# Optimization experiments

Hardware: AMD Instinct MI355X
Metric: run time of the kernel (lower is better)

The kernel has to match this reference:

```python
import jax, jax.numpy as jnp
import numpy as np

B, N, K, D, H, L = 2, 2048, 256, 768, 256, 64
REL_PROP = 3
NUM_BUCKETS = 64


def _pair_scores(u, dist_feat, left_w, left_b, right_w, right_b, out_w, out_b):
    # OptFFpairs-style pairwise scorer: left(u)_i + right(u)_j + dist_emb -> relu -> out
    left = jnp.einsum('bkd,hd->bkh', u, left_w) + left_b    # [B,K,H]
    right = jnp.einsum('bkd,hd->bkh', u, right_w) + right_b  # [B,K,H]
    h = jax.nn.relu(left[:, :, None, :] + right[:, None, :, :] + dist_feat)  # [B,K,K,H]
    return jnp.einsum('bijh,lh->bijl', h, out_w) + out_b     # [B,K,K,L]


def setup_inputs():
    key = jax.random.key(0)
    ks = jax.random.split(key, 12)
    s = 0.02
    all_span_vecs = jax.random.normal(ks[0], (B, N, D), dtype=jnp.float32)
    span_vecs = jax.random.normal(ks[1], (B, K, D), dtype=jnp.float32)
    span_begin = jnp.sort(jax.random.randint(ks[2], (B, K), 0, 1000), axis=-1).astype(jnp.int32)
    span_end = (span_begin + jax.random.randint(ks[3], (B, K), 1, 16)).astype(jnp.int32)
    square_mask = jnp.ones((B, K, K), dtype=jnp.float32)
    span_lengths = jnp.full((B,), float(K), dtype=jnp.float32)
    prune_indices = jnp.stack([
        jnp.sort(jax.random.choice(jax.random.fold_in(ks[4], b), N, (K,), replace=False))
        for b in range(B)
    ]).astype(jnp.int32)
    return {
        'all_span_vecs': all_span_vecs, 'span_vecs': span_vecs,
        'span_begin': span_begin, 'span_end': span_end,
        'square_mask': square_mask, 'span_lengths': span_lengths,
        'prune_indices': prune_indices,
        'left_w': jax.random.normal(ks[5], (H, D)) * s, 'left_b': jnp.zeros((H,), jnp.float32),
        'right_w': jax.random.normal(ks[6], (H, D)) * s, 'right_b': jnp.zeros((H,), jnp.float32),
        'dist_emb': jax.random.normal(ks[7], (NUM_BUCKETS, H)) * s,
        'out_w': jax.random.normal(ks[8], (L, H)) * s, 'out_b': jnp.zeros((L,), jnp.float32),
        'A_w': jax.random.normal(ks[9], (D, L)) * s,
        'B_w': jax.random.normal(ks[10], (D, L)) * s,
        'gate_w': jax.random.normal(ks[11], (D, 2 * D)) * s, 'gate_b': jnp.zeros((D,), jnp.float32),
    }


def reference(all_span_vecs, span_vecs, span_begin, span_end, square_mask, span_lengths,
              prune_indices, left_w, left_b, right_w, right_b, dist_emb, out_w, out_b,
              A_w, B_w, gate_w, gate_b):
    # distance-bucket embedding of the span pair (span_pair_generator)
    dist = span_begin[:, None, :] - span_end[:, :, None]                 # [B,K,K]
    buckets = jnp.clip(jnp.abs(dist), 0, NUM_BUCKETS - 1)
    dist_feat = dist_emb[buckets]                                        # [B,K,K,H]
    inv_len = 1.0 / span_lengths[:, None, None]                          # [B,1,1]

    update = span_vecs
    scores = _pair_scores(update, dist_feat, left_w, left_b, right_w, right_b, out_w, out_b)
    for _ in range(REL_PROP):
        probs = jax.nn.sigmoid(scores) * square_mask[..., None]          # [B,K,K,L]
        # torch: (A(probs) * update.unsqueeze(-2)).sum(-3) -> sum over i (rows)
        ctxt1 = jnp.einsum('bijl,dl,bid->bjd', probs, A_w, update) * inv_len
        # torch: (B(probs) * update.unsqueeze(-3)).sum(-2) -> sum over j (cols)
        ctxt2 = jnp.einsum('bijl,dl,bjd->bid', probs, B_w, update) * inv_len
        c = ctxt1 + ctxt2
        # MyGate: sigmoid-gated convex combination of old state and context
        g = jax.nn.sigmoid(jnp.concatenate([update, c], axis=-1) @ gate_w.T + gate_b)
        update = g * update + (1.0 - g) * c
        scores = _pair_scores(update, dist_feat, left_w, left_b, right_w, right_b, out_w, out_b)

    # overwrite_spans: scatter updated filtered spans back into the full span tensor
    valid = jnp.arange(K)[None, :] < span_lengths[:, None]               # [B,K]
    old = jnp.take_along_axis(all_span_vecs, prune_indices[..., None], axis=1)
    vals = jnp.where(valid[..., None], update, old)
    bidx = jnp.arange(B)[:, None]
    new_all = all_span_vecs.at[bidx, prune_indices].set(vals)
    return new_all, update, scores
```

## Files before the change

kernel.cpp:

```cpp
#include <hip/hip_runtime.h>

#define B_ 2
#define N_ 2048
#define K_ 256
#define D_ 768
#define H_ 256
#define L_ 64
#define BK_ (B_*K_)

typedef __attribute__((ext_vector_type(8))) __bf16 bf16x8;
typedef __attribute__((ext_vector_type(8))) unsigned short ushort8;
typedef __attribute__((ext_vector_type(4))) unsigned short ushort4v;
typedef __attribute__((ext_vector_type(4))) float f32x4;

__device__ __forceinline__ float sigm(float x) { return 1.0f / (1.0f + __expf(-x)); }

__device__ __forceinline__ unsigned short f2b(float f) {
    union { float f; unsigned int u; } v; v.f = f;
    unsigned int u = v.u;
    return (unsigned short)((u + 0x7FFFu + ((u >> 16) & 1u)) >> 16);
}
__device__ __forceinline__ unsigned short f2bc(float f) {
    __bf16 h = (__bf16)f;
    return __builtin_bit_cast(unsigned short, h);
}
__device__ __forceinline__ float b2f(unsigned short us) {
    union { unsigned int u; float f; } v; v.u = ((unsigned int)us) << 16;
    return v.f;
}
__device__ __forceinline__ bf16x8 ldb(const unsigned short* p) {
    ushort8 v = *(const ushort8*)p;
    return __builtin_bit_cast(bf16x8, v);
}

__global__ __launch_bounds__(256) void conv_all(
    const float* __restrict__ lw, const float* __restrict__ rw,
    const float* __restrict__ ow, const float* __restrict__ gw,
    const float* __restrict__ aw, const float* __restrict__ bw,
    const float* __restrict__ sv,
    unsigned short* __restrict__ lwb, unsigned short* __restrict__ rwb,
    unsigned short* __restrict__ owb, unsigned short* __restrict__ gwb,
    unsigned short* __restrict__ wab, unsigned short* __restrict__ wbb,
    unsigned short* __restrict__ ub)
{
    int i4 = (blockIdx.x * 256 + threadIdx.x) * 4;
    const float* src; unsigned short* dst; int off;
    if      (i4 <  196608) { src = lw; dst = lwb; off = 0; }
    else if (i4 <  393216) { src = rw; dst = rwb; off = 196608; }
    else if (i4 <  409600) { src = ow; dst = owb; off = 393216; }
    else if (i4 < 1589248) { src = gw; dst = gwb; off = 409600; }
    else if (i4 < 1638400) { src = aw; dst = wab; off = 1589248; }
    else if (i4 < 1687552) { src = bw; dst = wbb; off = 1638400; }
    else if (i4 < 2080768) { src = sv; dst = ub;  off = 1687552; }
    else return;
    int j = i4 - off;
    float4 v = *(const float4*)&src[j];
    ushort4v p; p.x = f2b(v.x); p.y = f2b(v.y); p.z = f2b(v.z); p.w = f2b(v.w);
    *(ushort4v*)&dst[j] = p;
}

__global__ __launch_bounds__(256) void conv_c(
    const float* __restrict__ c, unsigned short* __restrict__ cb)
{
    int i = (blockIdx.x * 256 + threadIdx.x) * 4;
    float4 v = *(const float4*)&c[i];
    ushort4v p; p.x = f2b(v.x); p.y = f2b(v.y); p.z = f2b(v.z); p.w = f2b(v.w);
    *(ushort4v*)&cb[i] = p;
}

__global__ __launch_bounds__(64) void lr_mfma2(
    const unsigned short* __restrict__ Ub,
    const unsigned short* __restrict__ lwb, const float* __restrict__ lb,
    const unsigned short* __restrict__ rwb, const float* __restrict__ rb,
    float* __restrict__ outL, float* __restrict__ outR)
{
    const int side = blockIdx.z;
    const unsigned short* __restrict__ W = side ? rwb : lwb;
    const float* __restrict__ bias = side ? rb : lb;
    float* __restrict__ outp = side ? outR : outL;
    const int r0 = blockIdx.x * 16, n0 = blockIdx.y * 16;
    const int lane = threadIdx.x;
    const int col = lane & 15, quad = lane >> 4;
    const unsigned short* arow = &Ub[(size_t)(r0 + col)*D_ + quad*8];
    const unsigned short* brow = &W[(size_t)(n0 + col)*D_ + quad*8];
    f32x4 acc = {};
    #pragma unroll
    for (int kc = 0; kc < D_; kc += 32) {
        bf16x8 a = ldb(arow + kc);
        bf16x8 bb = ldb(brow + kc);
        acc = __builtin_amdgcn_mfma_f32_16x16x32_bf16(a, bb, acc, 0, 0, 0);
    }
    const int n = n0 + col;
    const float bv = bias[n];
    #pragma unroll
    for (int r = 0; r < 4; ++r)
        outp[(size_t)(r0 + quad*4 + r)*H_ + n] = acc[r] + bv;
}

__global__ __launch_bounds__(256) void scores_v10(
    const float* __restrict__ leftb, const float* __restrict__ rightb,
    const int* __restrict__ span_begin, const int* __restrict__ span_end,
    const float* __restrict__ de, const unsigned short* __restrict__ owb,
    const float* __restrict__ out_b, const float* __restrict__ mask,
    float* __restrict__ S, unsigned short* __restrict__ Pt, int writeP)
{
    const int j0 = blockIdx.x * 64;
    const int i0 = blockIdx.y * 4;
    const int b  = blockIdx.z;
    const int tid = threadIdx.x;
    const int w = tid >> 6, lane = tid & 63, col = lane & 15, quad = lane >> 4;
    const int jrow = w*16 + col;

    __shared__ float sL[4][256];
    __shared__ float sT[64][68];
    __shared__ float sMask[4][64];
    __shared__ int   sBkt[4][64];

    {
        int ii = tid >> 6, jj = tid & 63;
        int d = span_begin[b*K_ + j0 + jj] - span_end[b*K_ + i0 + ii];
        if (d < 0) d = -d;
        sBkt[ii][jj] = d > 63 ? 63 : d;
        sMask[ii][jj] = mask[(size_t)(b*K_ + i0 + ii)*K_ + j0 + jj];
    }
    {
        int row = tid >> 6, c4 = (tid & 63) * 4;
        *(float4*)&sL[row][c4] = *(const float4*)&leftb[(size_t)(b*K_ + i0 + row)*H_ + c4];
    }
    __syncthreads();

    int deoff[4];
    #pragma unroll
    for (int i = 0; i < 4; ++i) deoff[i] = sBkt[i][jrow] * H_;

    const float* rrow = &rightb[(size_t)(b*K_ + j0 + jrow)*H_ + quad*8];

    f32x4 acc[4][4] = {};
    #pragma unroll
    for (int k = 0; k < 8; ++k) {
        const float4 r0 = *(const float4*)&rrow[k*32];
        const float4 r1 = *(const float4*)&rrow[k*32 + 4];
        bf16x8 bbk[4];
        #pragma unroll
        for (int lt = 0; lt < 4; ++lt)
            bbk[lt] = ldb(&owb[(size_t)(lt*16 + col)*H_ + k*32 + quad*8]);
        #pragma unroll
        for (int i = 0; i < 4; ++i) {
            const float* dr = &de[deoff[i] + k*32 + quad*8];
            const float4 d0 = *(const float4*)dr;
            const float4 d1 = *(const float4*)(dr + 4);
            const float* lr = &sL[i][k*32 + quad*8];
            const float4 l0 = *(const float4*)lr;
            const float4 l1 = *(const float4*)(lr + 4);
            bf16x8 a;
            a[0] = (__bf16)fmaxf(0.f, l0.x + r0.x + d0.x);
            a[1] = (__bf16)fmaxf(0.f, l0.y + r0.y + d0.y);
            a[2] = (__bf16)fmaxf(0.f, l0.z + r0.z + d0.z);
            a[3] = (__bf16)fmaxf(0.f, l0.w + r0.w + d0.w);
            a[4] = (__bf16)fmaxf(0.f, l1.x + r1.x + d1.x);
            a[5] = (__bf16)fmaxf(0.f, l1.y + r1.y + d1.y);
            a[6] = (__bf16)fmaxf(0.f, l1.z + r1.z + d1.z);
            a[7] = (__bf16)fmaxf(0.f, l1.w + r1.w + d1.w);
            #pragma unroll
            for (int lt = 0; lt < 4; ++lt)
                acc[i][lt] = __builtin_amdgcn_mfma_f32_16x16x32_bf16(a, bbk[lt], acc[i][lt], 0, 0, 0);
        }
    }

    float ob[4];
    #pragma unroll
    for (int lt = 0; lt < 4; ++lt) ob[lt] = out_b[lt*16 + col];

    #pragma unroll
    for (int i = 0; i < 4; ++i) {
        __syncthreads();
        #pragma unroll
        for (int lt = 0; lt < 4; ++lt)
            #pragma unroll
            for (int r = 0; r < 4; ++r)
                sT[w*16 + quad*4 + r][lt*16 + col] = acc[i][lt][r] + ob[lt];
        __syncthreads();
        const int jj = tid >> 2, seg = (tid & 3) * 16;
        const int j = j0 + jj, ii = i0 + i;
        if (writeP) {
            const float msk = sMask[i][jj];
            ushort8 o0, o1;
            #pragma unroll
            for (int e = 0; e < 8; ++e) {
                o0[e] = f2bc(sigm(sT[jj][seg + e]) * msk);
                o1[e] = f2bc(sigm(sT[jj][seg + 8 + e]) * msk);
            }
            unsigned short* dst = &Pt[(((size_t)b*K_ + j)*K_ + ii)*L_ + seg];
            *(ushort8*)&dst[0] = o0;
            *(ushort8*)&dst[8] = o1;
        } else {
            float* dst = &S[(((size_t)b*K_ + ii)*K_ + j)*L_ + seg];
            #pragma unroll
            for (int q2 = 0; q2 < 4; ++q2) {
                float4 v;
                v.x = sT[jj][seg + q2*4 + 0];
                v.y = sT[jj][seg + q2*4 + 1];
                v.z = sT[jj][seg + q2*4 + 2];
                v.w = sT[jj][seg + q2*4 + 3];
                *(float4*)&dst[q2*4] = v;
            }
        }
    }
}

__global__ __launch_bounds__(512, 4) void ctxt_v7(
    const unsigned short* __restrict__ Pt, const float* __restrict__ U,
    const unsigned short* __restrict__ WAb, const unsigned short* __restrict__ WBb,
    const float* __restrict__ lens, float* __restrict__ cacc)
{
    const int bid = blockIdx.x;
    const int m0 = (bid & 15) << 4;
    const int t0 = ((bid >> 4) & 7) << 5;
    const int mode = (bid >> 7) & 1;
    const int b = bid >> 8;
    const unsigned short* __restrict__ Wb = mode ? WBb : WAb;
    const int tid = threadIdx.x;
    const int w = tid >> 6, lane = tid & 63, col = lane & 15, quad = lane >> 4;
    const int dbase = w * 96;

    __shared__ unsigned short sP[2][16][72];
    __shared__ float sU[2][768];

    bf16x8 bw[6][2];
    #pragma unroll
    for (int dt = 0; dt < 6; ++dt)
        #pragma unroll
        for (int kc = 0; kc < 2; ++kc)
            bw[dt][kc] = ldb(&Wb[(size_t)(dbase + dt*16 + col)*L_ + kc*32 + quad*8]);

    const bool doP = tid < 128;
    const bool doU = (tid >= 128) && (tid < 320);
    const int prow = (tid & 127) >> 3, pseg = (tid & 7) * 8;
    const int ucol = (tid - 128) * 4;
    size_t pbase, tstep;
    if (mode) { pbase = (((size_t)b*K_ + t0)*K_ + m0 + prow)*L_ + pseg; tstep = (size_t)K_*L_; }
    else      { pbase = (((size_t)b*K_ + m0 + prow)*K_ + t0)*L_ + pseg; tstep = (size_t)L_; }

    ushort8 pvA, pvB; float4 uvA, uvB;
    if (doP) { pvA = *(const ushort8*)&Pt[pbase];
               pvB = *(const ushort8*)&Pt[pbase + tstep]; }
    if (doU) { uvA = *(const float4*)&U[((size_t)b*K_ + t0)*D_ + ucol];
               uvB = *(const float4*)&U[((size_t)b*K_ + t0 + 1)*D_ + ucol]; }

    f32x4 acc[6] = {};

    #define CTXT_COMPUTE(BUFI)                                                    \
    {                                                                             \
        bf16x8 a0 = ldb(&sP[BUFI][col][quad*8]);                                  \
        bf16x8 a1 = ldb(&sP[BUFI][col][32 + quad*8]);                             \
        _Pragma("unroll")                                                         \
        for (int dt = 0; dt < 6; ++dt) {                                          \
            f32x4 g = {0.f, 0.f, 0.f, 0.f};                                       \
            g = __builtin_amdgcn_mfma_f32_16x16x32_bf16(a0, bw[dt][0], g, 0, 0, 0); \
            g = __builtin_amdgcn_mfma_f32_16x16x32_bf16(a1, bw[dt][1], g, 0, 0, 0); \
            const float uu = sU[BUFI][dbase + dt*16 + col];                       \
            acc[dt] += g * uu;                                                    \
        }                                                                         \
    }

    for (int t = 0; t < 32; t += 2) {
        if (doP) *(ushort8*)&sP[0][prow][pseg] = pvA;
        if (doU) *(float4*)&sU[0][ucol] = uvA;
        __syncthreads();
        if (t + 2 < 32) {
            if (doP) pvA = *(const ushort8*)&Pt[pbase + (size_t)(t + 2)*tstep];
            if (doU) uvA = *(const float4*)&U[((size_t)b*K_ + t0 + t + 2)*D_ + ucol];
        }
        CTXT_COMPUTE(0)
        if (doP) *(ushort8*)&sP[1][prow][pseg] = pvB;
        if (doU) *(float4*)&sU[1][ucol] = uvB;
        __syncthreads();
        if (t + 3 < 32) {
            if (doP) pvB = *(const ushort8*)&Pt[pbase + (size_t)(t + 3)*tstep];
            if (doU) uvB = *(const float4*)&U[((size_t)b*K_ + t0 + t + 3)*D_ + ucol];
        }
        CTXT_COMPUTE(1)
    }
    #undef CTXT_COMPUTE

    const float inv_len = 1.0f / lens[b];
    #pragma unroll
    for (int dt = 0; dt < 6; ++dt)
        #pragma unroll
        for (int r = 0; r < 4; ++r) {
            const int m = m0 + quad*4 + r;
            atomicAdd(&cacc[((size_t)(b*K_) + m)*D_ + dbase + dt*16 + col],
                      acc[dt][r] * inv_len);
        }
}

__global__ __launch_bounds__(64) void gate_mfma2(
    const unsigned short* __restrict__ Ub, const unsigned short* __restrict__ cb,
    const unsigned short* __restrict__ gwb, const float* __restrict__ gb,
    const float* __restrict__ Ucur, const float* __restrict__ Cc,
    float* __restrict__ Unext, unsigned short* __restrict__ Ubnext)
{
    const int r0 = blockIdx.x * 16, n0 = blockIdx.y * 16;
    const int lane = threadIdx.x;
    const int col = lane & 15, quad = lane >> 4;
    const unsigned short* arow_u = &Ub[(size_t)(r0 + col)*D_ + quad*8];
    const unsigned short* arow_c = &cb[(size_t)(r0 + col)*D_ + quad*8];
    const unsigned short* brow   = &gwb[(size_t)(n0 + col)*(2*D_) + quad*8];
    f32x4 acc = {};
    #pragma unroll
    for (int kc = 0; kc < D_; kc += 32) {
        bf16x8 a = ldb(arow_u + kc);
        bf16x8 bb = ldb(brow + kc);
        acc = __builtin_amdgcn_mfma_f32_16x16x32_bf16(a, bb, acc, 0, 0, 0);
    }
    #pragma unroll
    for (int kc = 0; kc < D_; kc += 32) {
        bf16x8 a = ldb(arow_c + kc);
        bf16x8 bb = ldb(brow + D_ + kc);
        acc = __builtin_amdgcn_mfma_f32_16x16x32_bf16(a, bb, acc, 0, 0, 0);
    }
    const int n = n0 + col;
    const float gbv = gb[n];
    #pragma unroll
    for (int r = 0; r < 4; ++r) {
        const size_t idx = (size_t)(r0 + quad*4 + r)*D_ + n;
        const float gg = sigm(acc[r] + gbv);
        const float o = gg * Ucur[idx] + (1.f - gg) * Cc[idx];
        Unext[idx] = o;
        Ubnext[idx] = f2b(o);
    }
}

__global__ __launch_bounds__(256) void scatter_kernel(
    const float* __restrict__ upd, const int* __restrict__ prune,
    const float* __restrict__ lens, float* __restrict__ out_all)
{
    const int blk = blockIdx.x;
    const int b = blk / K_, k = blk % K_;
    if ((float)k < lens[b]) {
        const int pi = prune[b*K_ + k];
        const int tid = threadIdx.x;
        if (tid < D_/4) {
            float4 v = *(const float4*)&upd[((size_t)b*K_ + k)*D_ + tid*4];
            *(float4*)&out_all[((size_t)b*N_ + pi)*D_ + tid*4] = v;
        }
    }
}

extern "C" void kernel_launch(void* const* d_in, const int* in_sizes, int n_in,
                              void* d_out, int out_size, void* d_ws, size_t ws_size,
                              hipStream_t stream) {
    (void)in_sizes; (void)n_in; (void)out_size; (void)ws_size;
    const float* all_span_vecs = (const float*)d_in[0];
    const float* span_vecs     = (const float*)d_in[1];
    const int*   span_begin    = (const int*)d_in[2];
    const int*   span_end      = (const int*)d_in[3];
    const float* mask          = (const float*)d_in[4];
    const float* lens          = (const float*)d_in[5];
    const int*   prune         = (const int*)d_in[6];
    const float* lw  = (const float*)d_in[7];
    const float* lb  = (const float*)d_in[8];
    const float* rw  = (const float*)d_in[9];
    const float* rb  = (const float*)d_in[10];
    const float* dist_emb = (const float*)d_in[11];
    const float* out_w    = (const float*)d_in[12];
    const float* out_b    = (const float*)d_in[13];
    const float* A_w = (const float*)d_in[14];
    const float* B_w = (const float*)d_in[15];
    const float* gw  = (const float*)d_in[16];
    const float* gb  = (const float*)d_in[17];

    float* out_all = (float*)d_out;
    float* out_upd = out_all + (size_t)B_*N_*D_;
    float* out_sc  = out_upd + (size_t)BK_*D_;

    float* ws     = (float*)d_ws;
    float* leftb  = ws;
    float* rightf = leftb + (size_t)BK_*H_;
    float* U0     = rightf + (size_t)BK_*H_;
    float* U1     = U0 + (size_t)BK_*D_;
    float* cbuf   = U1 + (size_t)BK_*D_;
    unsigned short* WAb = (unsigned short*)(cbuf + (size_t)BK_*D_);
    unsigned short* WBb = WAb + (size_t)D_*L_;
    unsigned short* lwb = WBb + (size_t)D_*L_;
    unsigned short* rwb = lwb + (size_t)H_*D_;
    unsigned short* owb = rwb + (size_t)H_*D_;
    unsigned short* gwb = owb + (size_t)L_*H_;
    unsigned short* Ub0 = gwb + (size_t)D_*2*D_;
    unsigned short* Ub1 = Ub0 + (size_t)BK_*D_;
    unsigned short* cb  = Ub1 + (size_t)BK_*D_;
    unsigned short* Pt  = cb + (size_t)BK_*D_;

    hipMemcpyAsync(out_all, all_span_vecs, sizeof(float)*(size_t)B_*N_*D_,
                   hipMemcpyDeviceToDevice, stream);

    dim3 blk256(256), blk64(64), blk512(512);
    conv_all<<<dim3(2032), blk256, 0, stream>>>(lw, rw, out_w, gw, A_w, B_w, span_vecs,
                                                lwb, rwb, owb, gwb, WAb, WBb, Ub0);
    lr_mfma2<<<dim3(BK_/16, H_/16, 2), blk64, 0, stream>>>(Ub0, lwb, lb, rwb, rb, leftb, rightf);
    scores_v10<<<dim3(K_/64, K_/4, B_), blk256, 0, stream>>>(leftb, rightf, span_begin, span_end,
                                                             dist_emb, owb, out_b, mask,
                                                             out_sc, Pt, 1);
    const float* Ucur = span_vecs;
    const unsigned short* Ubcur = Ub0;
    float* nexts[3] = {U0, U1, out_upd};
    unsigned short* nextsUb[3] = {Ub1, Ub0, Ub1};
    for (int it = 0; it < 3; ++it) {
        hipMemsetAsync(cbuf, 0, sizeof(float)*(size_t)BK_*D_, stream);
        ctxt_v7<<<dim3(512), blk512, 0, stream>>>(Pt, Ucur, WAb, WBb, lens, cbuf);
        conv_c<<<dim3(BK_*D_/1024), blk256, 0, stream>>>(cbuf, cb);
        gate_mfma2<<<dim3(BK_/16, D_/16), blk64, 0, stream>>>(Ubcur, cb, gwb, gb,
                                                              Ucur, cbuf, nexts[it], nextsUb[it]);
        Ucur = nexts[it];
        Ubcur = nextsUb[it];
        lr_mfma2<<<dim3(BK_/16, H_/16, 2), blk64, 0, stream>>>(Ubcur, lwb, lb, rwb, rb, leftb, rightf);
        scores_v10<<<dim3(K_/64, K_/4, B_), blk256, 0, stream>>>(leftb, rightf, span_begin, span_end,
                                                                 dist_emb, owb, out_b, mask,
                                                                 out_sc, Pt, it == 2 ? 0 : 1);
    }
    scatter_kernel<<<dim3(BK_), blk256, 0, stream>>>(out_upd, prune, lens, out_all);
}
```

Before: 451.5 us.

## Write probabilities in both layouts and load MFMA fragments directly from global

The scores kernel now writes the sigmoid probabilities twice, once j-major and once i-major, so each ctxt mode can read contiguous 16x64 fragments. The ctxt kernel drops its shared-memory double buffering and barriers and loads the P fragments and U values straight from global memory. This aims to remove the strided loads and the synchronization cost. In exchange, scores writes twice as much P data, the workspace needs a second large buffer, and ctxt loses explicit prefetching and relies on the cache instead.

```diff
diff --git a/kernel.cpp b/kernel.cpp
--- a/kernel.cpp
+++ b/kernel.cpp
@@ -97,12 +97,13 @@
         outp[(size_t)(r0 + quad*4 + r)*H_ + n] = acc[r] + bv;
 }
 
-__global__ __launch_bounds__(256) void scores_v10(
+__global__ __launch_bounds__(256) void scores_v11(
     const float* __restrict__ leftb, const float* __restrict__ rightb,
     const int* __restrict__ span_begin, const int* __restrict__ span_end,
     const float* __restrict__ de, const unsigned short* __restrict__ owb,
     const float* __restrict__ out_b, const float* __restrict__ mask,
-    float* __restrict__ S, unsigned short* __restrict__ Pt, int writeP)
+    float* __restrict__ S, unsigned short* __restrict__ Pt,
+    unsigned short* __restrict__ Pt2, int writeP)
 {
     const int j0 = blockIdx.x * 64;
     const int i0 = blockIdx.y * 4;
@@ -193,6 +194,9 @@
             unsigned short* dst = &Pt[(((size_t)b*K_ + j)*K_ + ii)*L_ + seg];
             *(ushort8*)&dst[0] = o0;
             *(ushort8*)&dst[8] = o1;
+            unsigned short* dst2 = &Pt2[(((size_t)b*K_ + ii)*K_ + j)*L_ + seg];
+            *(ushort8*)&dst2[0] = o0;
+            *(ushort8*)&dst2[8] = o1;
         } else {
             float* dst = &S[(((size_t)b*K_ + ii)*K_ + j)*L_ + seg];
             #pragma unroll
@@ -208,8 +212,9 @@
     }
 }
 
-__global__ __launch_bounds__(512, 4) void ctxt_v7(
-    const unsigned short* __restrict__ Pt, const float* __restrict__ U,
+__global__ __launch_bounds__(512, 4) void ctxt_v8(
+    const unsigned short* __restrict__ Pt, const unsigned short* __restrict__ Pt2,
+    const float* __restrict__ U,
     const unsigned short* __restrict__ WAb, const unsigned short* __restrict__ WBb,
     const float* __restrict__ lens, float* __restrict__ cacc)
 {
@@ -218,14 +223,12 @@
     const int t0 = ((bid >> 4) & 7) << 5;
     const int mode = (bid >> 7) & 1;
     const int b = bid >> 8;
-    const unsigned short* __restrict__ Wb = mode ? WBb : WAb;
+    const unsigned short* __restrict__ Wb    = mode ? WBb : WAb;
+    const unsigned short* __restrict__ Pbase = mode ? Pt  : Pt2;
     const int tid = threadIdx.x;
     const int w = tid >> 6, lane = tid & 63, col = lane & 15, quad = lane >> 4;
     const int dbase = w * 96;
 
-    __shared__ unsigned short sP[2][16][72];
-    __shared__ float sU[2][768];
-
     bf16x8 bw[6][2];
     #pragma unroll
     for (int dt = 0; dt < 6; ++dt)
@@ -233,55 +236,23 @@
         for (int kc = 0; kc < 2; ++kc)
             bw[dt][kc] = ldb(&Wb[(size_t)(dbase + dt*16 + col)*L_ + kc*32 + quad*8]);
 
-    const bool doP = tid < 128;
-    const bool doU = (tid >= 128) && (tid < 320);
-    const int prow = (tid & 127) >> 3, pseg = (tid & 7) * 8;
-    const int ucol = (tid - 128) * 4;
-    size_t pbase, tstep;
-    if (mode) { pbase = (((size_t)b*K_ + t0)*K_ + m0 + prow)*L_ + pseg; tstep = (size_t)K_*L_; }
-    else      { pbase = (((size_t)b*K_ + m0 + prow)*K_ + t0)*L_ + pseg; tstep = (size_t)L_; }
-
-    ushort8 pvA, pvB; float4 uvA, uvB;
-    if (doP) { pvA = *(const ushort8*)&Pt[pbase];
-               pvB = *(const ushort8*)&Pt[pbase + tstep]; }
-    if (doU) { uvA = *(const float4*)&U[((size_t)b*K_ + t0)*D_ + ucol];
-               uvB = *(const float4*)&U[((size_t)b*K_ + t0 + 1)*D_ + ucol]; }
-
+    const size_t fragoff = (size_t)col*L_ + quad*8;
     f32x4 acc[6] = {};
-
-    #define CTXT_COMPUTE(BUFI)                                                    \
-    {                                                                             \
-        bf16x8 a0 = ldb(&sP[BUFI][col][quad*8]);                                  \
-        bf16x8 a1 = ldb(&sP[BUFI][col][32 + quad*8]);                             \
-        _Pragma("unroll")                                                         \
-        for (int dt = 0; dt < 6; ++dt) {                                          \
-            f32x4 g = {0.f, 0.f, 0.f, 0.f};                                       \
-            g = __builtin_amdgcn_mfma_f32_16x16x32_bf16(a0, bw[dt][0], g, 0, 0, 0); \
-            g = __builtin_amdgcn_mfma_f32_16x16x32_bf16(a1, bw[dt][1], g, 0, 0, 0); \
-            const float uu = sU[BUFI][dbase + dt*16 + col];                       \
-            acc[dt] += g * uu;                                                    \
-        }                                                                         \
-    }
-
-    for (int t = 0; t < 32; t += 2) {
-        if (doP) *(ushort8*)&sP[0][prow][pseg] = pvA;
-        if (doU) *(float4*)&sU[0][ucol] = uvA;
-        __syncthreads();
-        if (t + 2 < 32) {
-            if (doP) pvA = *(const ushort8*)&Pt[pbase + (size_t)(t + 2)*tstep];
-            if (doU) uvA = *(const float4*)&U[((size_t)b*K_ + t0 + t + 2)*D_ + ucol];
-        }
-        CTXT_COMPUTE(0)
-        if (doP) *(ushort8*)&sP[1][prow][pseg] = pvB;
-        if (doU) *(float4*)&sU[1][ucol] = uvB;
-        __syncthreads();
-        if (t + 3 < 32) {
-            if (doP) pvB = *(const ushort8*)&Pt[pbase + (size_t)(t + 3)*tstep];
-            if (doU) uvB = *(const float4*)&U[((size_t)b*K_ + t0 + t + 3)*D_ + ucol];
-        }
-        CTXT_COMPUTE(1)
-    }
-    #undef CTXT_COMPUTE
+    #pragma unroll 2
+    for (int t = 0; t < 32; ++t) {
+        const unsigned short* pA =
+            &Pbase[(((size_t)(b*K_ + t0 + t))*K_ + m0)*L_];
+        bf16x8 a0 = ldb(&pA[fragoff]);
+        bf16x8 a1 = ldb(&pA[fragoff + 32]);
+        const float* urow = &U[(size_t)(b*K_ + t0 + t)*D_ + dbase + col];
+        #pragma unroll
+        for (int dt = 0; dt < 6; ++dt) {
+            f32x4 g = {0.f, 0.f, 0.f, 0.f};
+            g = __builtin_amdgcn_mfma_f32_16x16x32_bf16(a0, bw[dt][0], g, 0, 0, 0);
+            g = __builtin_amdgcn_mfma_f32_16x16x32_bf16(a1, bw[dt][1], g, 0, 0, 0);
+            acc[dt] += g * urow[dt*16];
+        }
+    }
 
     const float inv_len = 1.0f / lens[b];
     #pragma unroll
@@ -390,6 +361,7 @@
     unsigned short* Ub1 = Ub0 + (size_t)BK_*D_;
     unsigned short* cb  = Ub1 + (size_t)BK_*D_;
     unsigned short* Pt  = cb + (size_t)BK_*D_;
+    unsigned short* Pt2 = Pt + (size_t)B_*K_*K_*L_;
 
     hipMemcpyAsync(out_all, all_span_vecs, sizeof(float)*(size_t)B_*N_*D_,
                    hipMemcpyDeviceToDevice, stream);
@@ -398,25 +370,25 @@
     conv_all<<<dim3(2032), blk256, 0, stream>>>(lw, rw, out_w, gw, A_w, B_w, span_vecs,
                                                 lwb, rwb, owb, gwb, WAb, WBb, Ub0);
     lr_mfma2<<<dim3(BK_/16, H_/16, 2), blk64, 0, stream>>>(Ub0, lwb, lb, rwb, rb, leftb, rightf);
-    scores_v10<<<dim3(K_/64, K_/4, B_), blk256, 0, stream>>>(leftb, rightf, span_begin, span_end,
+    scores_v11<<<dim3(K_/64, K_/4, B_), blk256, 0, stream>>>(leftb, rightf, span_begin, span_end,
                                                              dist_emb, owb, out_b, mask,
-                                                             out_sc, Pt, 1);
+                                                             out_sc, Pt, Pt2, 1);
     const float* Ucur = span_vecs;
     const unsigned short* Ubcur = Ub0;
     float* nexts[3] = {U0, U1, out_upd};
     unsigned short* nextsUb[3] = {Ub1, Ub0, Ub1};
     for (int it = 0; it < 3; ++it) {
         hipMemsetAsync(cbuf, 0, sizeof(float)*(size_t)BK_*D_, stream);
-        ctxt_v7<<<dim3(512), blk512, 0, stream>>>(Pt, Ucur, WAb, WBb, lens, cbuf);
+        ctxt_v8<<<dim3(512), blk512, 0, stream>>>(Pt, Pt2, Ucur, WAb, WBb, lens, cbuf);
         conv_c<<<dim3(BK_*D_/1024), blk256, 0, stream>>>(cbuf, cb);
         gate_mfma2<<<dim3(BK_/16, D_/16), blk64, 0, stream>>>(Ubcur, cb, gwb, gb,
                                                               Ucur, cbuf, nexts[it], nextsUb[it]);
         Ucur = nexts[it];
         Ubcur = nextsUb[it];
         lr_mfma2<<<dim3(BK_/16, H_/16, 2), blk64, 0, stream>>>(Ubcur, lwb, lb, rwb, rb, leftb, rightf);
-        scores_v10<<<dim3(K_/64, K_/4, B_), blk256, 0, stream>>>(leftb, rightf, span_begin, span_end,
+        scores_v11<<<dim3(K_/64, K_/4, B_), blk256, 0, stream>>>(leftb, rightf, span_begin, span_end,
                                                                  dist_emb, owb, out_b, mask,
-                                                                 out_sc, Pt, it == 2 ? 0 : 1);
+                                                                 out_sc, Pt, Pt2, it == 2 ? 0 : 1);
     }
     scatter_kernel<<<dim3(BK_), blk256, 0, stream>>>(out_upd, prune, lens, out_all);
 }
```

New measurement: 535.3 us. +18.6%, slower.
